# Optimization experiments

Hardware: AMD Instinct MI355X
Metric: run time of the kernel (lower is better)

Reference implementation:

```python
import jax, jax.numpy as jnp
import numpy as np

D = 16          # input_dim (no augmentations)
HID = 256       # hidden_dim
WIN = 64        # window_size
LEN = 1000      # len_noise
INTU = 50       # len_interval_u
B = 512
PAIRS = D * (D - 1) // 2      # 120 depth-2 Lyndon pairs
LOGSIG = D + PAIRS            # 136 logsignature channels


def _static_schedule():
    """Replicates compute_multilevel_logsignature's index logic on static times."""
    tb = np.linspace(0.0, 1.0, LEN)
    tu = tb[::INTU]
    tt = np.linspace(0.0, 1.0, WIN)
    u_indices = np.searchsorted(tb, tu, side='right') - 1
    t_indices = np.searchsorted(tb, tt[1:], side='right') - 1
    u_idx_for_t = np.searchsorted(tu, tt[1:], side='right') - 1
    start_idx = u_indices[np.maximum(u_idx_for_t, 0)]
    # build u_logsigrnn times and the per-step last_h update mask
    qt, last = [], -1
    for iu in u_idx_for_t:
        iu = max(int(iu), 0)
        if iu != last:
            qt.append(tu[iu]); last = iu
    qt.append(tt[-1])
    upd = np.zeros(WIN, dtype=bool)
    for i, t in enumerate(tt):
        if qt and t >= qt[0]:
            qt.pop(0); upd[i] = True
    return tb, t_indices, start_idx, upd


def setup_inputs() -> dict:
    key = jax.random.key(0)
    ks = jax.random.split(key, 6)
    def lin(k, fo, fi):  # kaiming-style fan_in init
        return jax.random.normal(k, (fo, fi), jnp.float32) * np.float32(np.sqrt(2.0 / fi))
    return {
        "z": jax.random.normal(ks[0], (B, LEN, D), jnp.float32),
        "W1": lin(ks[1], HID, HID + LOGSIG), "b1": jnp.zeros((HID,), jnp.float32),
        "W2": lin(ks[2], HID, HID),          "b2": jnp.zeros((HID,), jnp.float32),
        "W3": lin(ks[3], HID, HID),          "b3": jnp.zeros((HID,), jnp.float32),
        "W_lin": lin(ks[4], HID, HID),
    }


def reference(z, W1, b1, W2, b2, W3, b3, W_lin):
    tb, t_idx, s_idx, upd = _static_schedule()
    # Brownian path: z[:,0]=0, z[:,1:] *= sqrt(dt), cumsum
    dt_sqrt = jnp.sqrt(jnp.asarray(np.diff(tb), jnp.float32))          # [LEN-1]
    z = jnp.concatenate([jnp.zeros_like(z[:, :1]), z[:, 1:] * dt_sqrt[None, :, None]], axis=1)
    X = jnp.cumsum(z, axis=1)                                           # [B,LEN,D]
    # depth-2 logsignature with basepoint=0: level1 = X[end]; level2 = Levy area
    iu, ju = np.triu_indices(D, 1)
    Xp, dX = X[:, :-1], X[:, 1:] - X[:, :-1]
    pair = Xp[..., iu] * dX[..., ju] - Xp[..., ju] * dX[..., iu]        # [B,LEN-1,PAIRS]
    C = jnp.concatenate([jnp.zeros_like(pair[:, :1]), jnp.cumsum(pair, axis=1)], axis=1)
    lvl1 = X[:, t_idx]
    levy = 0.5 * (C[:, t_idx] - C[:, s_idx])
    logsig = jnp.concatenate([lvl1, levy], axis=-1)
    logsig = jnp.concatenate([jnp.zeros_like(logsig[:, :1]), logsig], axis=1)  # prepend zeros
    seq = jnp.moveaxis(logsig, 1, 0)

    def mlp(v):  # FeedForwardNN([hid,hid]) + Tanh
        v = jax.nn.relu(v @ W1.T + b1)
        v = jax.nn.relu(v @ W2.T + b2)
        return jnp.tanh(v @ W3.T + b3)

    def step(last_h, xs):
        ls, u = xs
        h = mlp(jnp.concatenate([last_h, ls], axis=-1))
        new_last = jnp.where(u, h, last_h)
        return new_last, h @ W_lin.T

    h0 = jnp.zeros((z.shape[0], HID), z.dtype)  # init_fixed=True
    _, ys = jax.lax.scan(step, h0, (seq, jnp.asarray(upd)))
    return jnp.moveaxis(ys, 0, 1)
```

## Files before the change

kernel.cpp:

```cpp
#include <hip/hip_runtime.h>
#include <hip/hip_bf16.h>
#include <cmath>
#include <cstring>

#define B_SZ   512
#define SLEN   1000
#define DD     16
#define HID    256
#define WIN    64
#define PAIRS  120
#define LSIG   136
#define NWIN   20
#define MAXST  21
#define K1P    416
#define W1FN   (13 * 16 * 64 * 8)
#define WFN    (8 * 16 * 64 * 8)
#define PSTEP  21

using short8  = __attribute__((ext_vector_type(8))) short;
using short4v = __attribute__((ext_vector_type(4))) short;
using half8   = __attribute__((ext_vector_type(8))) _Float16;
using f32x4   = __attribute__((ext_vector_type(4))) float;

struct SchedArgs { short snapk[SLEN - 1]; };
struct CombPArgs { unsigned char winofm[WIN]; unsigned char zl[WIN]; unsigned char sstep[WIN]; };
struct ChainArgs { int nsteps; unsigned char kU[32]; };
struct FuseArgs  { unsigned char sidx[WIN]; };

__device__ __forceinline__ unsigned short f2h(float x) {
  _Float16 h = (_Float16)x;
  return __builtin_bit_cast(unsigned short, h);
}
__device__ __forceinline__ float ftanh(float x) {
  float t = fminf(fmaxf(2.f * x, -30.f), 30.f);
  float e = __expf(t);
  return (e - 1.f) / (e + 1.f);
}

__global__ __launch_bounds__(128) void prep_kernel(
    const float* __restrict__ z,
    const float* __restrict__ W1, const float* __restrict__ W2,
    const float* __restrict__ W3, const float* __restrict__ Wl,
    float* __restrict__ logsig, float* __restrict__ dxwin,
    unsigned short* __restrict__ W1f, unsigned short* __restrict__ W2f,
    unsigned short* __restrict__ W3f, unsigned short* __restrict__ Wlf,
    SchedArgs A)
{
  const int w = blockIdx.x, b = blockIdx.y, tid = threadIdx.x;
  if (w >= NWIN) {
    const int slot = ((w - NWIN) * B_SZ + b) * 128 + tid;
    for (int e = slot; e < W1FN + 3 * WFN; e += 3 * B_SZ * 128) {
      if (e < W1FN) {
        int f = e;
        int j = f & 7, l15 = (f >> 3) & 15, lq = (f >> 7) & 3, nsub = (f >> 9) & 15, kk = f >> 13;
        int row = nsub * 16 + l15, col = kk * 32 + lq * 8 + j;
        float v = (col < HID + LSIG) ? W1[(size_t)row * (HID + LSIG) + col] : 0.f;
        W1f[f] = f2h(v);
      } else {
        int e2 = e - W1FN;
        int which = e2 >> 16, f = e2 & 65535;
        int j = f & 7, l15 = (f >> 3) & 15, lq = (f >> 7) & 3, nsub = (f >> 9) & 15, kk = (f >> 13) & 7;
        int row = nsub * 16 + l15, col = kk * 32 + lq * 8 + j;
        const float* src = which == 0 ? W2 : which == 1 ? W3 : Wl;
        unsigned short* dst = which == 0 ? W2f : which == 1 ? W3f : Wlf;
        dst[f] = f2h(src[(size_t)row * HID + col]);
      }
    }
    return;
  }
  __shared__ float zs[50][16];
  const int ns = (w == NWIN - 1) ? 49 : 50;
  const float* src = z + ((size_t)b * SLEN + 50 * w + 1) * DD;
  const double s999 = 1.0 / (double)(SLEN - 1);
  for (int c = tid; c < ns * 4; c += 128) {
    float4 v = ((const float4*)src)[c];
    int t = 50 * w + (c >> 2);
    double a = (t + 1 == SLEN - 1) ? 1.0 : (double)(t + 1) * s999;
    float s = sqrtf((float)(a - (double)t * s999));
    v.x *= s; v.y *= s; v.z *= s; v.w *= s;
    ((float4*)&zs[0][0])[c] = v;
  }
  int pi = 0, pj = 0;
  if (tid < PAIRS) { int rem = tid, i = 0; while (rem >= DD - 1 - i) { rem -= DD - 1 - i; ++i; } pi = i; pj = i + 1 + rem; }
  __syncthreads();
  float Yi = 0.f, Yj = 0.f, LL = 0.f, Yd = 0.f;
  const int base_t = 50 * w;
  for (int u = 0; u < ns; ++u) {
    const float di = zs[u][pi], dj = zs[u][pj];
    LL = fmaf(Yi, dj, LL); LL = fmaf(-Yj, di, LL);
    Yi += di; Yj += dj;
    if (tid < DD) Yd += zs[u][tid];
    const int m = A.snapk[base_t + u];
    if (m) {
      float* dst = logsig + ((size_t)b * WIN + m) * LSIG;
      if (tid < DD)    dst[tid]      = Yd;
      if (tid < PAIRS) dst[DD + tid] = LL;
    }
  }
  if (tid < DD) dxwin[((size_t)b * NWIN + w) * DD + tid] = Yd;
}

__global__ __launch_bounds__(256) void combp_kernel(
    float* __restrict__ logsig, const float* __restrict__ dxwin,
    const unsigned short* __restrict__ W1f, const float* __restrict__ b1,
    float* __restrict__ partial, CombPArgs A)
{
  __shared__ float Xs[16][16], Yt[16][16];
  __shared__ __align__(16) unsigned short As[20 * 16 * 8];
  const int k = blockIdx.x, g = blockIdx.y, tid = threadIdx.x;
  const int w = A.winofm[k], zl = A.zl[k], ss = A.sstep[k];
  for (int c = tid; c < 3 * 16 * 8; c += 256) As[17 * 16 * 8 + c] = 0;
  {
    const int bi = tid >> 4, col = tid & 15;
    const size_t b = (size_t)(g * 16 + bi);
    float acc = 0.f;
    for (int ww = 0; ww < w; ++ww) acc += dxwin[(b * NWIN + ww) * DD + col];
    float y = (k == 0) ? 0.f : logsig[(b * WIN + k) * LSIG + col];
    float fin = (k == 0) ? 0.f : acc + y;
    Xs[bi][col] = acc; Yt[bi][col] = y;
    logsig[(b * WIN + k) * LSIG + col] = fin;
    As[((col >> 3) * 16 + bi) * 8 + (col & 7)] = f2h(fin);
  }
  __syncthreads();
  for (int idx = tid; idx < 16 * PAIRS; idx += 256) {
    const int bi = idx / PAIRS, p = idx - bi * PAIRS;
    int rem = p, i = 0; while (rem >= DD - 1 - i) { rem -= DD - 1 - i; ++i; }
    const int pi = i, pj = i + 1 + rem;
    const size_t b = (size_t)(g * 16 + bi);
    float ll = (k == 0) ? 0.f : logsig[(b * WIN + k) * LSIG + DD + p];
    float fin = (k == 0 || zl) ? 0.f
              : 0.5f * (ll + Xs[bi][pi] * Yt[bi][pj] - Xs[bi][pj] * Yt[bi][pi]);
    logsig[(b * WIN + k) * LSIG + DD + p] = fin;
    const int c = DD + p;
    As[((c >> 3) * 16 + bi) * 8 + (c & 7)] = f2h(fin);
  }
  if (ss == 255) return;
  __syncthreads();
  const int lane = tid & 63, wv = tid >> 6;
  const int l15 = lane & 15, lq = lane >> 4;
  f32x4 acc4[4] = {{0,0,0,0},{0,0,0,0},{0,0,0,0},{0,0,0,0}};
#pragma unroll
  for (int kt = 0; kt < 5; ++kt) {
    half8 af = *(const half8*)&As[((kt * 4 + lq) * 16 + l15) * 8];
#pragma unroll
    for (int t = 0; t < 4; ++t) {
      half8 bfW = *(const half8*)(W1f + ((size_t)((8 + kt) * 16 + wv * 4 + t) * 64 + lane) * 8);
      acc4[t] = __builtin_amdgcn_mfma_f32_16x16x32_f16(bfW, af, acc4[t], 0, 0, 0);
    }
  }
#pragma unroll
  for (int t = 0; t < 4; ++t) {
    const int col0 = wv * 64 + t * 16 + lq * 4;
    f32x4 bb = *(const f32x4*)(b1 + col0);
    f32x4 r = acc4[t] + bb;
    *(f32x4*)&partial[(((size_t)g * PSTEP + ss) * 16 + l15) * HID + col0] = r;
  }
}

__global__ __attribute__((amdgpu_flat_work_group_size(512, 512)))
__attribute__((amdgpu_waves_per_eu(2, 2)))
void chain_kernel(
    const float* __restrict__ partial,
    const unsigned short* __restrict__ W1f, const unsigned short* __restrict__ W2f,
    const unsigned short* __restrict__ W3f,
    const float* __restrict__ b2, const float* __restrict__ b3,
    unsigned short* __restrict__ statesb, ChainArgs A)
{
  __shared__ __align__(16) unsigned short A0s[32 * 16 * 8];
  __shared__ __align__(16) unsigned short A1s[32 * 16 * 8];
  __shared__ __align__(16) unsigned short A2s[32 * 16 * 8];
  const int tid = threadIdx.x, g = blockIdx.x;
  const int lane = tid & 63, w = tid >> 6;
  const int l15 = lane & 15, lq = lane >> 4;

  for (int c = tid; c < 32 * 16 * 8; c += 512) A0s[c] = 0;
  for (int c = tid; c < 16 * HID / 4; c += 512) {
    int r = c >> 6, col = (c & 63) * 4;
    *(short4v*)&statesb[((size_t)(g * 16 + r) * MAXST + 0) * HID + col] = (short4v){0, 0, 0, 0};
  }

  half8 W1r[16], W2r[16], W3r[16];
#pragma unroll
  for (int kk = 0; kk < 8; ++kk)
#pragma unroll
    for (int nt = 0; nt < 2; ++nt) {
      W1r[kk * 2 + nt] = *(const half8*)(W1f + ((size_t)(kk * 16 + w * 2 + nt) * 64 + lane) * 8);
      W2r[kk * 2 + nt] = *(const half8*)(W2f + ((size_t)(kk * 16 + w * 2 + nt) * 64 + lane) * 8);
      W3r[kk * 2 + nt] = *(const half8*)(W3f + ((size_t)(kk * 16 + w * 2 + nt) * 64 + lane) * 8);
    }

  int colb[2];
  f32x4 bias2v[2], bias3v[2];
#pragma unroll
  for (int nt = 0; nt < 2; ++nt) {
    colb[nt] = w * 32 + nt * 16 + lq * 4;
    bias2v[nt] = *(const f32x4*)(b2 + colb[nt]);
    bias3v[nt] = *(const f32x4*)(b3 + colb[nt]);
  }

  const float* pbase = partial + (size_t)g * PSTEP * 16 * HID;
  int poff[2];
#pragma unroll
  for (int nt = 0; nt < 2; ++nt) poff[nt] = l15 * HID + colb[nt];
  f32x4 pf[2];
  pf[0] = *(const f32x4*)(pbase + poff[0]);
  pf[1] = *(const f32x4*)(pbase + poff[1]);

  short4v hv4[2];
  __syncthreads();

  for (int m = 0; m < A.nsteps; ++m) {
    if (m > 0) {
#pragma unroll
      for (int nt = 0; nt < 2; ++nt)
        *(short4v*)&statesb[((size_t)(g * 16 + l15) * MAXST + m) * HID + colb[nt]] = hv4[nt];
    }
    {
      f32x4 acc[2][2];
      acc[0][0] = pf[0]; acc[0][1] = pf[1];
      acc[1][0] = (f32x4){0.f,0.f,0.f,0.f}; acc[1][1] = (f32x4){0.f,0.f,0.f,0.f};
      if (m + 1 < A.nsteps) {
        const float* pp = pbase + (size_t)(m + 1) * 16 * HID;
        pf[0] = *(const f32x4*)(pp + poff[0]);
        pf[1] = *(const f32x4*)(pp + poff[1]);
      }
#pragma unroll
      for (int kk = 0; kk < 8; ++kk) {
        half8 af = *(const half8*)&A0s[((kk * 4 + lq) * 16 + l15) * 8];
        acc[kk & 1][0] = __builtin_amdgcn_mfma_f32_16x16x32_f16(W1r[kk * 2    ], af, acc[kk & 1][0], 0, 0, 0);
        acc[kk & 1][1] = __builtin_amdgcn_mfma_f32_16x16x32_f16(W1r[kk * 2 + 1], af, acc[kk & 1][1], 0, 0, 0);
      }
#pragma unroll
      for (int nt = 0; nt < 2; ++nt) {
        f32x4 s = acc[0][nt] + acc[1][nt];
        short4v h4;
#pragma unroll
        for (int r4 = 0; r4 < 4; ++r4) h4[r4] = (short)f2h(fmaxf(s[r4], 0.f));
        *(short4v*)&A1s[((colb[nt] >> 3) * 16 + l15) * 8 + (colb[nt] & 7)] = h4;
      }
    }
    __syncthreads();
    {
      f32x4 acc[2][2] = {{{0.f,0.f,0.f,0.f},{0.f,0.f,0.f,0.f}},{{0.f,0.f,0.f,0.f},{0.f,0.f,0.f,0.f}}};
#pragma unroll
      for (int kk = 0; kk < 8; ++kk) {
        half8 af = *(const half8*)&A1s[((kk * 4 + lq) * 16 + l15) * 8];
        acc[kk & 1][0] = __builtin_amdgcn_mfma_f32_16x16x32_f16(W2r[kk * 2    ], af, acc[kk & 1][0], 0, 0, 0);
        acc[kk & 1][1] = __builtin_amdgcn_mfma_f32_16x16x32_f16(W2r[kk * 2 + 1], af, acc[kk & 1][1], 0, 0, 0);
      }
#pragma unroll
      for (int nt = 0; nt < 2; ++nt) {
        f32x4 s = acc[0][nt] + acc[1][nt] + bias2v[nt];
        short4v h4;
#pragma unroll
        for (int r4 = 0; r4 < 4; ++r4) h4[r4] = (short)f2h(fmaxf(s[r4], 0.f));
        *(short4v*)&A2s[((colb[nt] >> 3) * 16 + l15) * 8 + (colb[nt] & 7)] = h4;
      }
    }
    __syncthreads();
    {
      f32x4 acc[2][2] = {{{0.f,0.f,0.f,0.f},{0.f,0.f,0.f,0.f}},{{0.f,0.f,0.f,0.f},{0.f,0.f,0.f,0.f}}};
#pragma unroll
      for (int kk = 0; kk < 8; ++kk) {
        half8 af = *(const half8*)&A2s[((kk * 4 + lq) * 16 + l15) * 8];
        acc[kk & 1][0] = __builtin_amdgcn_mfma_f32_16x16x32_f16(W3r[kk * 2    ], af, acc[kk & 1][0], 0, 0, 0);
        acc[kk & 1][1] = __builtin_amdgcn_mfma_f32_16x16x32_f16(W3r[kk * 2 + 1], af, acc[kk & 1][1], 0, 0, 0);
      }
#pragma unroll
      for (int nt = 0; nt < 2; ++nt) {
        f32x4 s = acc[0][nt] + acc[1][nt] + bias3v[nt];
        short4v h4;
#pragma unroll
        for (int r4 = 0; r4 < 4; ++r4) h4[r4] = (short)f2h(ftanh(s[r4]));
        hv4[nt] = h4;
        *(short4v*)&A0s[((colb[nt] >> 3) * 16 + l15) * 8 + (colb[nt] & 7)] = h4;
      }
    }
    __syncthreads();
  }
  {
    const int m = A.nsteps;
#pragma unroll
    for (int nt = 0; nt < 2; ++nt)
      *(short4v*)&statesb[((size_t)(g * 16 + l15) * MAXST + m) * HID + colb[nt]] = hv4[nt];
  }
}

__global__ __launch_bounds__(256, 3) void fused_kernel(
    const unsigned short* __restrict__ statesb, const float* __restrict__ logsig,
    const unsigned short* __restrict__ W1f, const unsigned short* __restrict__ W2f,
    const unsigned short* __restrict__ W3f, const unsigned short* __restrict__ Wlf,
    const float* __restrict__ b1, const float* __restrict__ b2, const float* __restrict__ b3,
    float* __restrict__ out, FuseArgs F)
{
  __shared__ __align__(16) unsigned short act[32 * 64 * 8];
  __shared__ __align__(16) unsigned short atile[2][4 * 64 * 8];
  const int tid = threadIdx.x, b = blockIdx.x;
  const int lane = tid & 63, w = tid >> 6;
  const int l15 = lane & 15, lq = lane >> 4;

  f32x4 acc[4][4];
#pragma unroll
  for (int a = 0; a < 4; ++a)
#pragma unroll
    for (int t = 0; t < 4; ++t) acc[a][t] = (f32x4){0.f, 0.f, 0.f, 0.f};

  const int lr = tid >> 2, lcc = (tid & 3) * 8;
  short8 pk;
  auto loadA = [&](int kk) {
    int col = kk * 32 + lcc;
    if (col < HID) {
      pk = *(const short8*)(statesb + ((size_t)b * MAXST + F.sidx[lr]) * HID + col);
    } else {
      const float* sp = logsig + ((size_t)b * WIN + lr) * LSIG + (col - HID);
      float4 v0 = ((const float4*)sp)[0];
      float4 v1 = ((const float4*)sp)[1];
      short8 q;
      q[0] = (short)f2h(v0.x); q[1] = (short)f2h(v0.y); q[2] = (short)f2h(v0.z); q[3] = (short)f2h(v0.w);
      q[4] = (short)f2h(v1.x); q[5] = (short)f2h(v1.y); q[6] = (short)f2h(v1.z); q[7] = (short)f2h(v1.w);
      pk = q;
    }
  };
  loadA(0);
  for (int kk = 0; kk < 13; ++kk) {
    unsigned short* buf = &atile[kk & 1][0];
    *(short8*)&buf[((lcc >> 3) * 64 + lr) * 8] = pk;
    __syncthreads();
    if (kk + 1 < 13) loadA(kk + 1);
    half8 bfr[4];
#pragma unroll
    for (int t = 0; t < 4; ++t)
      bfr[t] = *(const half8*)(W1f + ((size_t)(kk * 16 + w * 4 + t) * 64 + lane) * 8);
#pragma unroll
    for (int a = 0; a < 4; ++a) {
      half8 af = *(const half8*)&buf[(lq * 64 + a * 16 + l15) * 8];
#pragma unroll
      for (int t = 0; t < 4; ++t)
        acc[a][t] = __builtin_amdgcn_mfma_f32_16x16x32_f16(bfr[t], af, acc[a][t], 0, 0, 0);
    }
  }
#pragma unroll
  for (int t = 0; t < 4; ++t) {
    const int col0 = w * 64 + t * 16 + lq * 4;
    f32x4 bb = *(const f32x4*)(b1 + col0);
#pragma unroll
    for (int a = 0; a < 4; ++a) {
      const int row = a * 16 + l15;
      short4v h4;
#pragma unroll
      for (int r4 = 0; r4 < 4; ++r4) h4[r4] = (short)f2h(fmaxf(acc[a][t][r4] + bb[r4], 0.f));
      *(short4v*)&act[((col0 >> 3) * 64 + row) * 8 + (col0 & 7)] = h4;
    }
  }
  __syncthreads();

  auto layer = [&](const unsigned short* Wf) {
#pragma unroll
    for (int a = 0; a < 4; ++a)
#pragma unroll
      for (int t = 0; t < 4; ++t) acc[a][t] = (f32x4){0.f, 0.f, 0.f, 0.f};
    for (int kk = 0; kk < 8; ++kk) {
      half8 bfr[4];
#pragma unroll
      for (int t = 0; t < 4; ++t)
        bfr[t] = *(const half8*)(Wf + ((size_t)(kk * 16 + w * 4 + t) * 64 + lane) * 8);
#pragma unroll
      for (int a = 0; a < 4; ++a) {
        half8 af = *(const half8*)&act[((kk * 4 + lq) * 64 + a * 16 + l15) * 8];
#pragma unroll
        for (int t = 0; t < 4; ++t)
          acc[a][t] = __builtin_amdgcn_mfma_f32_16x16x32_f16(bfr[t], af, acc[a][t], 0, 0, 0);
      }
    }
  };

  layer(W2f);
  __syncthreads();
#pragma unroll
  for (int t = 0; t < 4; ++t) {
    const int col0 = w * 64 + t * 16 + lq * 4;
    f32x4 bb = *(const f32x4*)(b2 + col0);
#pragma unroll
    for (int a = 0; a < 4; ++a) {
      const int row = a * 16 + l15;
      short4v h4;
#pragma unroll
      for (int r4 = 0; r4 < 4; ++r4) h4[r4] = (short)f2h(fmaxf(acc[a][t][r4] + bb[r4], 0.f));
      *(short4v*)&act[((col0 >> 3) * 64 + row) * 8 + (col0 & 7)] = h4;
    }
  }
  __syncthreads();

  layer(W3f);
  __syncthreads();
#pragma unroll
  for (int t = 0; t < 4; ++t) {
    const int col0 = w * 64 + t * 16 + lq * 4;
    f32x4 bb = *(const f32x4*)(b3 + col0);
#pragma unroll
    for (int a = 0; a < 4; ++a) {
      const int row = a * 16 + l15;
      short4v h4;
#pragma unroll
      for (int r4 = 0; r4 < 4; ++r4) h4[r4] = (short)f2h(ftanh(acc[a][t][r4] + bb[r4]));
      *(short4v*)&act[((col0 >> 3) * 64 + row) * 8 + (col0 & 7)] = h4;
    }
  }
  __syncthreads();

  layer(Wlf);
#pragma unroll
  for (int t = 0; t < 4; ++t) {
    const int col0 = w * 64 + t * 16 + lq * 4;
#pragma unroll
    for (int a = 0; a < 4; ++a) {
      const int ks = a * 16 + l15;
      *(f32x4*)&out[((size_t)b * WIN + ks) * HID + col0] = acc[a][t];
    }
  }
}

static void build_sched(SchedArgs& P, CombPArgs& CB, ChainArgs& CH, FuseArgs& FU) {
  double tb[SLEN], tt[WIN], tu[NWIN];
  const double s999 = 1.0 / (double)(SLEN - 1);
  const double s63  = 1.0 / (double)(WIN - 1);
  for (int i = 0; i < SLEN; ++i) tb[i] = (double)i * s999;
  tb[SLEN - 1] = 1.0;
  for (int k = 0; k < WIN; ++k) tt[k] = (double)k * s63;
  tt[WIN - 1] = 1.0;
  for (int j = 0; j < NWIN; ++j) tu[j] = tb[50 * j];

  int t_idx[WIN - 1], u_for_t[WIN - 1];
  for (int k = 1; k < WIN; ++k) {
    int ii = 0;
    for (int q = 0; q < SLEN; ++q) if (tb[q] <= tt[k]) ii = q;
    t_idx[k - 1] = ii;
    int jj = 0;
    for (int q = 0; q < NWIN; ++q) if (tu[q] <= tt[k]) jj = q;
    u_for_t[k - 1] = jj;
  }
  for (int t = 0; t < SLEN - 1; ++t) P.snapk[t] = 0;
  for (int m = 1; m < WIN; ++m) P.snapk[t_idx[m - 1] - 1] = (short)m;

  for (int m = 0; m < WIN; ++m) { CB.winofm[m] = 0; CB.zl[m] = 0; CB.sstep[m] = 255; }
  for (int m = 1; m < WIN; ++m) {
    int p = t_idx[m - 1];
    CB.winofm[m] = (unsigned char)((p - 1) / 50);
    CB.zl[m] = (p % 50 == 0) ? 1 : 0;
  }

  double qt[32]; int nq = 0, last = -1;
  for (int m = 0; m < WIN - 1; ++m) {
    const int iu = u_for_t[m];
    if (iu != last) { qt[nq++] = tu[iu]; last = iu; }
  }
  qt[nq++] = tt[WIN - 1];
  int upd[WIN]; int qh = 0;
  for (int i = 0; i < WIN; ++i) {
    upd[i] = 0;
    if (qh < nq && tt[i] >= qt[qh]) { qh++; upd[i] = 1; }
  }
  int nU = 0;
  for (int k = 0; k < WIN; ++k) if (upd[k]) { if (nU < 32) CH.kU[nU] = (unsigned char)k; ++nU; }
  int cnt = 0;
  for (int k = 0; k < WIN; ++k) { FU.sidx[k] = (unsigned char)cnt; if (upd[k]) ++cnt; }
  CH.nsteps = FU.sidx[WIN - 1];
  for (int s = 0; s < nU && s < 32; ++s)
    if (s < PSTEP) CB.sstep[CH.kU[s]] = (unsigned char)s;
}

extern "C" void kernel_launch(void* const* d_in, const int* in_sizes, int n_in,
                              void* d_out, int out_size, void* d_ws, size_t ws_size,
                              hipStream_t stream) {
  const float* z  = (const float*)d_in[0];
  const float* W1 = (const float*)d_in[1];
  const float* b1 = (const float*)d_in[2];
  const float* W2 = (const float*)d_in[3];
  const float* b2 = (const float*)d_in[4];
  const float* W3 = (const float*)d_in[5];
  const float* b3 = (const float*)d_in[6];
  const float* Wl = (const float*)d_in[7];

  char* ws = (char*)d_ws;
  float* logsig = (float*)(ws);
  size_t o = (size_t)B_SZ * WIN * LSIG * 4;
  float* dxwin            = (float*)(ws + o); o += (size_t)B_SZ * NWIN * DD * 4;
  unsigned short* statesb = (unsigned short*)(ws + o); o += (size_t)B_SZ * MAXST * HID * 2;
  unsigned short* W1f     = (unsigned short*)(ws + o); o += (size_t)W1FN * 2;
  unsigned short* W2f     = (unsigned short*)(ws + o); o += (size_t)WFN * 2;
  unsigned short* W3f     = (unsigned short*)(ws + o); o += (size_t)WFN * 2;
  unsigned short* Wlf     = (unsigned short*)(ws + o); o += (size_t)WFN * 2;
  float* partial          = (float*)(ws + o); o += (size_t)32 * PSTEP * 16 * HID * 4;

  SchedArgs P; CombPArgs CB; ChainArgs CH; FuseArgs FU;
  build_sched(P, CB, CH, FU);

  prep_kernel<<<dim3(NWIN + 3, B_SZ), 128, 0, stream>>>(
      z, W1, W2, W3, Wl, logsig, dxwin, W1f, W2f, W3f, Wlf, P);
  combp_kernel<<<dim3(WIN, 32), 256, 0, stream>>>(logsig, dxwin, W1f, b1, partial, CB);
  chain_kernel<<<32, 512, 0, stream>>>(partial, W1f, W2f, W3f, b2, b3, statesb, CH);
  fused_kernel<<<512, 256, 0, stream>>>(statesb, logsig, W1f, W2f, W3f, Wlf,
                                        b1, b2, b3, (float*)d_out, FU);
}
```

Baseline: 220.0 us.

## Stage logsig in LDS once and load state fragments directly from global

The double-buffered shared A-tile, which needed a __syncthreads on every one of the 13 K-steps, is removed. The logsig part of the first-layer input is now converted to fp16 once and staged in LDS at kernel start. The hidden-state part is read as MFMA fragments straight from global memory using per-lane precomputed row offsets. This removes the per-step barrier and the LDS round trip for the state operand, but raises LDS use per block and depends on uncoalesced-ish direct global fragment loads hitting cache.

```diff
diff --git a/kernel.cpp b/kernel.cpp
--- a/kernel.cpp
+++ b/kernel.cpp
@@ -294,46 +294,48 @@
     float* __restrict__ out, FuseArgs F)
 {
   __shared__ __align__(16) unsigned short act[32 * 64 * 8];
-  __shared__ __align__(16) unsigned short atile[2][4 * 64 * 8];
+  __shared__ __align__(16) unsigned short lsig[20 * 64 * 8];
   const int tid = threadIdx.x, b = blockIdx.x;
   const int lane = tid & 63, w = tid >> 6;
   const int l15 = lane & 15, lq = lane >> 4;
 
+  {
+    const int srow = tid & 63, sq = tid >> 6;
+#pragma unroll
+    for (int j = 0; j < 10; ++j) {
+      const int c = (sq * 10 + j) * 4;
+      float4 v = *(const float4*)(logsig + ((size_t)b * WIN + srow) * LSIG + c);
+      short4v q;
+      q[0] = (short)f2h(v.x); q[1] = (short)f2h(v.y); q[2] = (short)f2h(v.z); q[3] = (short)f2h(v.w);
+      *(short4v*)&lsig[((c >> 3) * 64 + srow) * 8 + (c & 7)] = q;
+    }
+  }
+
   f32x4 acc[4][4];
 #pragma unroll
   for (int a = 0; a < 4; ++a)
 #pragma unroll
     for (int t = 0; t < 4; ++t) acc[a][t] = (f32x4){0.f, 0.f, 0.f, 0.f};
 
-  const int lr = tid >> 2, lcc = (tid & 3) * 8;
-  short8 pk;
-  auto loadA = [&](int kk) {
-    int col = kk * 32 + lcc;
-    if (col < HID) {
-      pk = *(const short8*)(statesb + ((size_t)b * MAXST + F.sidx[lr]) * HID + col);
-    } else {
-      const float* sp = logsig + ((size_t)b * WIN + lr) * LSIG + (col - HID);
-      float4 v0 = ((const float4*)sp)[0];
-      float4 v1 = ((const float4*)sp)[1];
-      short8 q;
-      q[0] = (short)f2h(v0.x); q[1] = (short)f2h(v0.y); q[2] = (short)f2h(v0.z); q[3] = (short)f2h(v0.w);
-      q[4] = (short)f2h(v1.x); q[5] = (short)f2h(v1.y); q[6] = (short)f2h(v1.z); q[7] = (short)f2h(v1.w);
-      pk = q;
-    }
-  };
-  loadA(0);
+  size_t srb[4];
+#pragma unroll
+  for (int a = 0; a < 4; ++a) {
+    const int ks = a * 16 + l15;
+    srb[a] = ((size_t)b * MAXST + F.sidx[ks]) * HID + lq * 8;
+  }
+  __syncthreads();
+
+#pragma unroll
   for (int kk = 0; kk < 13; ++kk) {
-    unsigned short* buf = &atile[kk & 1][0];
-    *(short8*)&buf[((lcc >> 3) * 64 + lr) * 8] = pk;
-    __syncthreads();
-    if (kk + 1 < 13) loadA(kk + 1);
     half8 bfr[4];
 #pragma unroll
     for (int t = 0; t < 4; ++t)
       bfr[t] = *(const half8*)(W1f + ((size_t)(kk * 16 + w * 4 + t) * 64 + lane) * 8);
 #pragma unroll
     for (int a = 0; a < 4; ++a) {
-      half8 af = *(const half8*)&buf[(lq * 64 + a * 16 + l15) * 8];
+      half8 af;
+      if (kk < 8) af = *(const half8*)(statesb + srb[a] + kk * 32);
+      else        af = *(const half8*)&lsig[(((kk - 8) * 4 + lq) * 64 + a * 16 + l15) * 8];
 #pragma unroll
       for (int t = 0; t < 4; ++t)
         acc[a][t] = __builtin_amdgcn_mfma_f32_16x16x32_f16(bfr[t], af, acc[a][t], 0, 0, 0);
```

Measured after the change: 223.6 us. Within noise of the previous version (+1.6%).
